# Optimization experiments

Measured on AMD Instinct MI355X. Metric: run time of the kernel, lower is better.

## Reference

```python
import jax, jax.numpy as jnp
import numpy as np

D_MODEL = 1024
N_HEADS = 16
N_KV_HEADS = 4
D_HEAD = D_MODEL // N_HEADS  # 64
GROUP = N_HEADS // N_KV_HEADS  # 4
SCALE = 1.0 / np.sqrt(D_HEAD)
BATCH, SEQ = 2, 2048


def setup_inputs() -> dict:
    key = jax.random.key(0)
    ks = jax.random.split(key, 12)
    w = 0.02
    qkv = jax.random.normal(ks[0], (BATCH, SEQ, D_MODEL), dtype=jnp.float32)
    # RoPE angles: positions * inverse frequencies, shape [SEQ, D_HEAD//2]
    inv_freq = 1.0 / (10000.0 ** (jnp.arange(0, D_HEAD, 2, dtype=jnp.float32) / D_HEAD))
    pos_emb = jnp.arange(SEQ, dtype=jnp.float32)[:, None] * inv_freq[None, :]
    Wq = jax.random.normal(ks[1], (D_MODEL, D_MODEL), dtype=jnp.float32) * w
    bq = jax.random.normal(ks[2], (D_MODEL,), dtype=jnp.float32) * w
    Wk = jax.random.normal(ks[3], (D_MODEL, N_KV_HEADS * D_HEAD), dtype=jnp.float32) * w
    bk = jax.random.normal(ks[4], (N_KV_HEADS * D_HEAD,), dtype=jnp.float32) * w
    Wv = jax.random.normal(ks[5], (D_MODEL, N_KV_HEADS * D_HEAD), dtype=jnp.float32) * w
    bv = jax.random.normal(ks[6], (N_KV_HEADS * D_HEAD,), dtype=jnp.float32) * w
    Wo = jax.random.normal(ks[7], (D_MODEL, D_MODEL), dtype=jnp.float32) * w
    bo = jax.random.normal(ks[8], (D_MODEL,), dtype=jnp.float32) * w
    return {"qkv": qkv, "pos_emb": pos_emb, "Wq": Wq, "bq": bq, "Wk": Wk, "bk": bk,
            "Wv": Wv, "bv": bv, "Wo": Wo, "bo": bo}


def _rotate_half(x):
    x1, x2 = jnp.split(x, 2, axis=-1)
    return jnp.concatenate([-x2, x1], axis=-1)


def _apply_rope(q, k, pos_emb):
    # q: [B,S,H,Dh], k: [B,S,Kv,Dh], pos_emb: [S, Dh/2] angles
    cos = jnp.cos(pos_emb)
    sin = jnp.sin(pos_emb)
    cos = jnp.concatenate([cos, cos], axis=-1)[None, :, None, :]  # [1,S,1,Dh]
    sin = jnp.concatenate([sin, sin], axis=-1)[None, :, None, :]
    q = q * cos + _rotate_half(q) * sin
    k = k * cos + _rotate_half(k) * sin
    return q, k


def reference(qkv, pos_emb, Wq, bq, Wk, bk, Wv, bv, Wo, bo):
    B, S, D = qkv.shape
    q = qkv @ Wq + bq                           # [B,S,D]
    k = qkv @ Wk + bk                           # [B,S,Kv*Dh]
    v = qkv @ Wv + bv
    q = q.reshape(B, S, N_HEADS, D_HEAD)
    k = k.reshape(B, S, N_KV_HEADS, D_HEAD)
    v = v.reshape(B, S, N_KV_HEADS, D_HEAD)
    q, k = _apply_rope(q, k, pos_emb)
    q = q.transpose(0, 2, 1, 3)                 # [B,H,S,Dh]
    k = k.transpose(0, 2, 1, 3)                 # [B,Kv,S,Dh]
    v = v.transpose(0, 2, 1, 3)
    # GQA: replicate each kv head across its query-head group
    k = jnp.repeat(k, GROUP, axis=1)            # [B,H,S,Dh]
    v = jnp.repeat(v, GROUP, axis=1)
    scores = jnp.einsum('bhqd,bhkd->bhqk', q, k) * SCALE
    causal = jnp.tril(jnp.ones((S, S), dtype=bool))
    scores = jnp.where(causal[None, None, :, :], scores, jnp.finfo(scores.dtype).min)
    attn = jax.nn.softmax(scores, axis=-1)
    out = jnp.einsum('bhqk,bhkd->bhqd', attn, v)  # [B,H,S,Dh]
    out = out.transpose(0, 2, 1, 3).reshape(B, S, D)
    return out @ Wo + bo
```

## Files before the change

kernel.cpp:

```cpp
#include <hip/hip_runtime.h>
#include <hip/hip_bf16.h>

using f32x4  = __attribute__((ext_vector_type(4))) float;
using short8 = __attribute__((ext_vector_type(8))) short;
using u16    = unsigned short;
using u32    = unsigned int;

#define B_SZ   2
#define S_LEN  2048
#define NH     16
#define NKV    4
#define DH     64
#define DM     1024
#define NQKVC  1536
#define MROWS  4096
#define QSCALE 0.18033688011112042f

__device__ __forceinline__ u16 f2bf(float f) {
  return __builtin_bit_cast(u16, __float2bfloat16(f));
}
__device__ __forceinline__ float bf2f(u16 b) {
  return __builtin_bit_cast(float, ((u32)b) << 16);
}
__device__ __forceinline__ void gld16(const void* g, void* l) {
  __builtin_amdgcn_global_load_lds((const __attribute__((address_space(1))) u32*)g,
                                   (__attribute__((address_space(3))) u32*)l, 16, 0, 0);
}

__device__ __forceinline__ void transp_tile(const float* __restrict__ w, int ncols,
                                            u16* __restrict__ wt, int bx, int by,
                                            int tid, float (*t)[33]) {
  const int k0 = bx * 32, n0 = by * 32;
  const int tx = tid & 31, ty = tid >> 5;
#pragma unroll
  for (int j = 0; j < 32; j += 8)
    t[ty + j][tx] = w[(size_t)(k0 + ty + j) * ncols + n0 + tx];
  __syncthreads();
#pragma unroll
  for (int j = 0; j < 32; j += 8)
    wt[(size_t)(n0 + ty + j) * 1024 + k0 + tx] = f2bf(t[tx][ty + j]);
}

__global__ __launch_bounds__(256) void k_prep(
    const float* __restrict__ x, u16* __restrict__ xb,
    const float* __restrict__ Wq, const float* __restrict__ Wk,
    const float* __restrict__ Wv, const float* __restrict__ Wo,
    u16* __restrict__ Wqkvt, u16* __restrict__ Wot,
    const float* __restrict__ bq, const float* __restrict__ bk,
    const float* __restrict__ bv, const float* __restrict__ pe,
    float* __restrict__ biasqkv, float* __restrict__ cs, float* __restrict__ sn) {
  __shared__ float tt[32][33];
  const int job = blockIdx.x, tid = threadIdx.x;
  if (job < 1024) {
#pragma unroll
    for (int u = 0; u < 4; ++u) {
      int i = job * 4096 + u * 1024 + tid * 4;
      float4 v = *(const float4*)(x + i);
      ushort4 o;
      o.x = f2bf(v.x); o.y = f2bf(v.y); o.z = f2bf(v.z); o.w = f2bf(v.w);
      *(ushort4*)(xb + i) = o;
    }
  } else if (job < 2048) {
    int t = job - 1024;
    transp_tile(Wq, 1024, Wqkvt, t & 31, t >> 5, tid, tt);
  } else if (job < 2304) {
    int t = job - 2048;
    transp_tile(Wk, 256, Wqkvt + (size_t)1024 * 1024, t & 31, t >> 5, tid, tt);
  } else if (job < 2560) {
    int t = job - 2304;
    transp_tile(Wv, 256, Wqkvt + (size_t)1280 * 1024, t & 31, t >> 5, tid, tt);
  } else if (job < 3584) {
    int t = job - 2560;
    transp_tile(Wo, 1024, Wot, t & 31, t >> 5, tid, tt);
  } else {
    int i = (job - 3584) * 256 + tid;
    if (i < NQKVC)
      biasqkv[i] = (i < 1024) ? bq[i] : (i < 1280 ? bk[i - 1024] : bv[i - 1280]);
    float a = pe[i];
    cs[i] = cosf(a);
    sn[i] = sinf(a);
  }
}

template <typename OUT_T>
__global__ __launch_bounds__(256) void k_gemm(const u16* __restrict__ A,
                                              const u16* __restrict__ Bt,
                                              const float* __restrict__ bias,
                                              OUT_T* __restrict__ C,
                                              int M, int N, int K) {
  __shared__ u16 la[128 * 32];
  __shared__ u16 lb[64 * 32];
  const int tid = threadIdx.x;
  const int m0 = blockIdx.x * 128, n0 = blockIdx.y * 64;
  const int lane = tid & 63, wv = tid >> 6;
  const int g = lane >> 4, lr = lane & 15;
  const int wr = wv >> 1, wc = wv & 1;

  const int sr = tid >> 2;
  const int scol = (tid & 3) * 8;
  const u16* pa0 = A  + (size_t)(m0 + sr) * K + scol;
  const u16* pa1 = A  + (size_t)(m0 + 64 + sr) * K + scol;
  const u16* pb  = Bt + (size_t)(n0 + sr) * K + scol;
  u16* lda0 = &la[wv * 512];
  u16* lda1 = &la[2048 + wv * 512];
  u16* ldb  = &lb[wv * 512];

  f32x4 acc[4][2] = {};
  const int nk = K >> 5;
  for (int kt = 0; kt < nk; ++kt) {
    const int ko = kt * 32;
    gld16(pa0 + ko, lda0);
    gld16(pa1 + ko, lda1);
    gld16(pb + ko, ldb);
    __syncthreads();
    short8 af[4], bfr[2];
#pragma unroll
    for (int m = 0; m < 4; ++m)
      af[m] = *(const short8*)&la[(64 * wr + 16 * m + lr) * 32 + 8 * g];
#pragma unroll
    for (int n = 0; n < 2; ++n)
      bfr[n] = *(const short8*)&lb[(32 * wc + 16 * n + lr) * 32 + 8 * g];
#pragma unroll
    for (int m = 0; m < 4; ++m)
#pragma unroll
      for (int n = 0; n < 2; ++n)
        acc[m][n] = __builtin_amdgcn_mfma_f32_16x16x32_bf16(af[m], bfr[n], acc[m][n], 0, 0, 0);
    __syncthreads();
  }

#pragma unroll
  for (int m = 0; m < 4; ++m)
#pragma unroll
    for (int n = 0; n < 2; ++n) {
      const int col = n0 + 32 * wc + 16 * n + lr;
      const float bz = bias[col];
#pragma unroll
      for (int r = 0; r < 4; ++r) {
        const int row = m0 + 64 * wr + 16 * m + 4 * g + r;
        float v = acc[m][n][r] + bz;
        if constexpr (sizeof(OUT_T) == 2) C[(size_t)row * N + col] = f2bf(v);
        else                              C[(size_t)row * N + col] = v;
      }
    }
}

__global__ __launch_bounds__(256) void k_rv(const u16* __restrict__ p,
                                            const float* __restrict__ cs,
                                            const float* __restrict__ sn,
                                            u16* __restrict__ Qr, u16* __restrict__ Kr,
                                            u16* __restrict__ Vt) {
  __shared__ u16 tt[32][33];
  const int job = blockIdx.x, tid = threadIdx.x;
  if (job < 4096) {
    const int row = job;
    const int b = row >> 11, s = row & 2047;
    const u16* pr = p + (size_t)row * NQKVC;
    const float* crow = cs + s * 32;
    const float* srow = sn + s * 32;
#pragma unroll
    for (int it = 0; it < 4; ++it) {
      int c = it * 256 + tid;
      int h = c >> 6, d = c & 63, j = d & 31;
      float x = bf2f(pr[c]);
      float y = bf2f(pr[c ^ 32]);
      float o = (x * crow[j] + (d < 32 ? -y : y) * srow[j]) * QSCALE;
      Qr[((size_t)(b * NH + h) * S_LEN + s) * DH + d] = f2bf(o);
    }
    {
      int c = 1024 + tid;
      int kvh = tid >> 6, d = tid & 63, j = d & 31;
      float x = bf2f(pr[c]);
      float y = bf2f(pr[c ^ 32]);
      float o = x * crow[j] + (d < 32 ? -y : y) * srow[j];
      Kr[((size_t)(b * NKV + kvh) * S_LEN + s) * DH + d] = f2bf(o);
    }
  } else {
    const int idx = job - 4096;
    const int st = (idx & 63) * 32;
    const int dt = ((idx >> 6) & 1) * 32;
    const int bkv = idx >> 7;
    const int b = bkv >> 2, kv = bkv & 3;
    const int tx = tid & 31, ty = tid >> 5;
#pragma unroll
    for (int j = 0; j < 32; j += 8)
      tt[ty + j][tx] = p[(size_t)(b * S_LEN + st + ty + j) * NQKVC + 1280 + kv * 64 + dt + tx];
    __syncthreads();
#pragma unroll
    for (int j = 0; j < 32; j += 8)
      Vt[((size_t)(b * NKV + kv) * DH + dt + ty + j) * S_LEN + st + tx] = tt[tx][ty + j];
  }
}

__global__ __launch_bounds__(512, 4) void k_attn(const u16* __restrict__ Qr,
                                                 const u16* __restrict__ Kr,
                                                 const u16* __restrict__ Vt,
                                                 u16* __restrict__ Og) {
  __shared__ u16 kbuf[2][4096];
  __shared__ u16 vbuf[2][4096];
  __shared__ u16 plds[8][16][72];

  const int tid = threadIdx.x, wv = tid >> 6, lane = tid & 63;
  const int g = lane >> 4, lr = lane & 15;
  const int wg = blockIdx.x;
  const int xcd = wg & 7, iw = wg >> 3;
  const int bh = xcd * 4 + (iw & 3);
  const int j = iw >> 2;
  const int pr = (j < 8) ? j : 23 - j;
  const int b = bh >> 4, h = bh & 15, kv = h >> 2;
  const int qt = (wv >> 2) ? (31 - pr) : pr;
  const int q0w = qt * 64 + (wv & 3) * 16;
  const int myq = q0w + lr;
  const int myNt = qt + 1;
  const int nt = 32 - pr;

  const u16* Kbase = Kr + (size_t)(b * NKV + kv) * S_LEN * DH;
  const u16* Vbase = Vt + (size_t)(b * NKV + kv) * DH * S_LEN;

  const int sr = tid >> 3;
  const int sc = tid & 7;
  const int ssw = sc ^ (sr & 7);
  const int rsw = lr & 7;
  u16* prow = &plds[wv][lr][0];

  const u16* Qb = Qr + ((size_t)(b * NH + h) * S_LEN + q0w) * DH;
  short8 qf0 = *(const short8*)(Qb + lr * DH + 8 * g);
  short8 qf1 = *(const short8*)(Qb + lr * DH + 32 + 8 * g);

  float m = -1e30f, l = 0.f;
  f32x4 accO[4] = {};
  const f32x4 z = {};

  gld16(Kbase + (size_t)sr * DH + ssw * 8,    &kbuf[0][wv * 512]);
  gld16(Vbase + (size_t)sr * S_LEN + ssw * 8, &vbuf[0][wv * 512]);
  __syncthreads();
  int buf = 0;
  for (int ti = 0; ti < nt; ++ti) {
    const int kb = ti * 64;
    if (ti + 1 < nt) {
      const int kn = kb + 64;
      gld16(Kbase + (size_t)(kn + sr) * DH + ssw * 8,   &kbuf[buf ^ 1][wv * 512]);
      gld16(Vbase + (size_t)sr * S_LEN + kn + ssw * 8,  &vbuf[buf ^ 1][wv * 512]);
    }
    if (ti < myNt) {
      const u16* kl = kbuf[buf];
      const u16* vl = vbuf[buf];
      short8 k0[4], k1[4];
#pragma unroll
      for (int t = 0; t < 4; ++t) {
        const int row = 16 * t + lr;
        k0[t] = *(const short8*)&kl[row * 64 + (g ^ rsw) * 8];
        k1[t] = *(const short8*)&kl[row * 64 + ((4 + g) ^ rsw) * 8];
      }
      f32x4 s[4];
      __builtin_amdgcn_s_setprio(1);
#pragma unroll
      for (int t = 0; t < 4; ++t) {
        s[t] = __builtin_amdgcn_mfma_f32_16x16x32_bf16(k0[t], qf0, z, 0, 0, 0);
        s[t] = __builtin_amdgcn_mfma_f32_16x16x32_bf16(k1[t], qf1, s[t], 0, 0, 0);
      }
      __builtin_amdgcn_s_setprio(0);
      if (kb + 63 > q0w) {
#pragma unroll
        for (int t = 0; t < 4; ++t)
#pragma unroll
          for (int r = 0; r < 4; ++r)
            if (kb + 16 * t + 4 * g + r > myq) s[t][r] = -1e30f;
      }
      float a0 = fmaxf(fmaxf(fmaxf(s[0][0], s[0][1]), s[0][2]), s[0][3]);
      float a1 = fmaxf(fmaxf(fmaxf(s[1][0], s[1][1]), s[1][2]), s[1][3]);
      float a2 = fmaxf(fmaxf(fmaxf(s[2][0], s[2][1]), s[2][2]), s[2][3]);
      float a3 = fmaxf(fmaxf(fmaxf(s[3][0], s[3][1]), s[3][2]), s[3][3]);
      float tm = fmaxf(fmaxf(a0, a1), fmaxf(a2, a3));
      tm = fmaxf(tm, __shfl_xor(tm, 16));
      tm = fmaxf(tm, __shfl_xor(tm, 32));
      if (__any(tm > m + 8.f)) {
        float mn = fmaxf(tm, m);
        float al = __builtin_exp2f(m - mn);
        m = mn;
        l *= al;
#pragma unroll
        for (int t = 0; t < 4; ++t) {
          accO[t][0] *= al; accO[t][1] *= al; accO[t][2] *= al; accO[t][3] *= al;
        }
      }
      float rs = 0.f;
#pragma unroll
      for (int t = 0; t < 4; ++t)
#pragma unroll
        for (int r = 0; r < 4; ++r) {
          float e = __builtin_exp2f(s[t][r] - m);
          s[t][r] = e;
          rs += e;
        }
      rs += __shfl_xor(rs, 16);
      rs += __shfl_xor(rs, 32);
      l += rs;
#pragma unroll
      for (int t = 0; t < 4; ++t) {
        u32 lo = (u32)f2bf(s[t][0]) | ((u32)f2bf(s[t][1]) << 16);
        u32 hi = (u32)f2bf(s[t][2]) | ((u32)f2bf(s[t][3]) << 16);
        uint2 w2; w2.x = lo; w2.y = hi;
        *(uint2*)(prow + 16 * t + 4 * g) = w2;
      }
      short8 pb0 = *(const short8*)(prow + 8 * g);
      short8 pb1 = *(const short8*)(prow + 32 + 8 * g);
      __builtin_amdgcn_s_setprio(1);
#pragma unroll
      for (int t = 0; t < 4; ++t) {
        const int row = 16 * t + lr;
        short8 vf0 = *(const short8*)&vl[row * 64 + (g ^ rsw) * 8];
        short8 vf1 = *(const short8*)&vl[row * 64 + ((4 + g) ^ rsw) * 8];
        accO[t] = __builtin_amdgcn_mfma_f32_16x16x32_bf16(vf0, pb0, accO[t], 0, 0, 0);
        accO[t] = __builtin_amdgcn_mfma_f32_16x16x32_bf16(vf1, pb1, accO[t], 0, 0, 0);
      }
      __builtin_amdgcn_s_setprio(0);
    }
    __syncthreads();
    buf ^= 1;
  }

  const float inv = 1.0f / l;
  u16* orow = Og + ((size_t)(b * S_LEN + q0w + lr)) * DM + h * DH;
#pragma unroll
  for (int t = 0; t < 4; ++t) {
    ushort4 o;
    o.x = f2bf(accO[t][0] * inv);
    o.y = f2bf(accO[t][1] * inv);
    o.z = f2bf(accO[t][2] * inv);
    o.w = f2bf(accO[t][3] * inv);
    *(ushort4*)(orow + 16 * t + 4 * g) = o;
  }
}

extern "C" void kernel_launch(void* const* d_in, const int* in_sizes, int n_in,
                              void* d_out, int out_size, void* d_ws, size_t ws_size,
                              hipStream_t stream) {
  const float* x  = (const float*)d_in[0];
  const float* pe = (const float*)d_in[1];
  const float* Wq = (const float*)d_in[2];
  const float* bq = (const float*)d_in[3];
  const float* Wk = (const float*)d_in[4];
  const float* bk = (const float*)d_in[5];
  const float* Wv = (const float*)d_in[6];
  const float* bv = (const float*)d_in[7];
  const float* Wo = (const float*)d_in[8];
  const float* bo = (const float*)d_in[9];
  float* out = (float*)d_out;

  char* w = (char*)d_ws;
  u16* Xb      = (u16*)w;   w += (size_t)MROWS * DM * 2;
  u16* Wqkvt   = (u16*)w;   w += (size_t)NQKVC * DM * 2;
  u16* Wot     = (u16*)w;   w += (size_t)DM * DM * 2;
  float* biasq = (float*)w; w += NQKVC * 4;
  float* cs    = (float*)w; w += S_LEN * 32 * 4;
  float* sn    = (float*)w; w += S_LEN * 32 * 4;
  u16* QKVp    = (u16*)w;   w += (size_t)MROWS * NQKVC * 2;
  u16* Qr      = (u16*)w;   w += (size_t)B_SZ * NH * S_LEN * DH * 2;
  u16* Kr      = (u16*)w;   w += (size_t)B_SZ * NKV * S_LEN * DH * 2;
  u16* Vt      = (u16*)w;   w += (size_t)B_SZ * NKV * DH * S_LEN * 2;
  u16* Og      = (u16*)w;

  k_prep<<<3840, 256, 0, stream>>>(x, Xb, Wq, Wk, Wv, Wo, Wqkvt, Wot,
                                   bq, bk, bv, pe, biasq, cs, sn);

  k_gemm<u16><<<dim3(MROWS / 128, NQKVC / 64), 256, 0, stream>>>(
      Xb, Wqkvt, biasq, QKVp, MROWS, NQKVC, DM);

  k_rv<<<4096 + 1024, 256, 0, stream>>>(QKVp, cs, sn, Qr, Kr, Vt);

  k_attn<<<512, 512, 0, stream>>>(Qr, Kr, Vt, Og);

  k_gemm<float><<<dim3(MROWS / 128, DM / 64), 256, 0, stream>>>(
      Og, Wot, bo, out, MROWS, DM, DM);
}
```

Baseline: 187.2 us.

## Fuse RoPE and V transpose into QKV GEMM epilogue, double-buffer GEMM LDS

Adds a mode to the GEMM kernel whose epilogue stages the tile in shared memory, applies RoPE and the Q scale, and writes Qr, Kr and transposed Vt directly. This removes the separate rope/transpose kernel and the intermediate QKV buffer round trip. The GEMM main loop also double-buffers LDS, prefetching the next K slice before the MFMAs with one barrier per step. Larger shared memory use may reduce occupancy.

```diff
diff --git a/kernel.cpp b/kernel.cpp
--- a/kernel.cpp
+++ b/kernel.cpp
@@ -82,14 +82,23 @@
   }
 }
 
-template <typename OUT_T>
+template <int MODE, typename OUT_T>
 __global__ __launch_bounds__(256) void k_gemm(const u16* __restrict__ A,
                                               const u16* __restrict__ Bt,
                                               const float* __restrict__ bias,
                                               OUT_T* __restrict__ C,
-                                              int M, int N, int K) {
-  __shared__ u16 la[128 * 32];
-  __shared__ u16 lb[64 * 32];
+                                              int M, int N, int K,
+                                              const float* __restrict__ cs,
+                                              const float* __restrict__ sn,
+                                              u16* __restrict__ Qr,
+                                              u16* __restrict__ Kr,
+                                              u16* __restrict__ Vt) {
+  __shared__ __align__(16) char smraw[33280];
+  u16* laB0 = (u16*)smraw;
+  u16* laB1 = (u16*)smraw + 4096;
+  u16* lbB0 = (u16*)(smraw + 16384);
+  u16* lbB1 = (u16*)(smraw + 16384) + 2048;
+
   const int tid = threadIdx.x;
   const int m0 = blockIdx.x * 128, n0 = blockIdx.y * 64;
   const int lane = tid & 63, wv = tid >> 6;
@@ -101,18 +110,24 @@
   const u16* pa0 = A  + (size_t)(m0 + sr) * K + scol;
   const u16* pa1 = A  + (size_t)(m0 + 64 + sr) * K + scol;
   const u16* pb  = Bt + (size_t)(n0 + sr) * K + scol;
-  u16* lda0 = &la[wv * 512];
-  u16* lda1 = &la[2048 + wv * 512];
-  u16* ldb  = &lb[wv * 512];
 
   f32x4 acc[4][2] = {};
   const int nk = K >> 5;
+  gld16(pa0, laB0 + wv * 512);
+  gld16(pa1, laB0 + 2048 + wv * 512);
+  gld16(pb,  lbB0 + wv * 512);
+  __syncthreads();
   for (int kt = 0; kt < nk; ++kt) {
-    const int ko = kt * 32;
-    gld16(pa0 + ko, lda0);
-    gld16(pa1 + ko, lda1);
-    gld16(pb + ko, ldb);
-    __syncthreads();
+    const u16* la = (kt & 1) ? laB1 : laB0;
+    const u16* lb = (kt & 1) ? lbB1 : lbB0;
+    if (kt + 1 < nk) {
+      u16* lan = (kt & 1) ? laB0 : laB1;
+      u16* lbn = (kt & 1) ? lbB0 : lbB1;
+      const int ko = (kt + 1) * 32;
+      gld16(pa0 + ko, lan + wv * 512);
+      gld16(pa1 + ko, lan + 2048 + wv * 512);
+      gld16(pb + ko,  lbn + wv * 512);
+    }
     short8 af[4], bfr[2];
 #pragma unroll
     for (int m = 0; m < 4; ++m)
@@ -128,66 +143,74 @@
     __syncthreads();
   }
 
-#pragma unroll
-  for (int m = 0; m < 4; ++m)
-#pragma unroll
-    for (int n = 0; n < 2; ++n) {
-      const int col = n0 + 32 * wc + 16 * n + lr;
-      const float bz = bias[col];
-#pragma unroll
-      for (int r = 0; r < 4; ++r) {
-        const int row = m0 + 64 * wr + 16 * m + 4 * g + r;
-        float v = acc[m][n][r] + bz;
-        if constexpr (sizeof(OUT_T) == 2) C[(size_t)row * N + col] = f2bf(v);
-        else                              C[(size_t)row * N + col] = v;
-      }
-    }
-}
-
-__global__ __launch_bounds__(256) void k_rv(const u16* __restrict__ p,
-                                            const float* __restrict__ cs,
-                                            const float* __restrict__ sn,
-                                            u16* __restrict__ Qr, u16* __restrict__ Kr,
-                                            u16* __restrict__ Vt) {
-  __shared__ u16 tt[32][33];
-  const int job = blockIdx.x, tid = threadIdx.x;
-  if (job < 4096) {
-    const int row = job;
-    const int b = row >> 11, s = row & 2047;
-    const u16* pr = p + (size_t)row * NQKVC;
-    const float* crow = cs + s * 32;
-    const float* srow = sn + s * 32;
-#pragma unroll
-    for (int it = 0; it < 4; ++it) {
-      int c = it * 256 + tid;
-      int h = c >> 6, d = c & 63, j = d & 31;
-      float x = bf2f(pr[c]);
-      float y = bf2f(pr[c ^ 32]);
-      float o = (x * crow[j] + (d < 32 ? -y : y) * srow[j]) * QSCALE;
-      Qr[((size_t)(b * NH + h) * S_LEN + s) * DH + d] = f2bf(o);
-    }
-    {
-      int c = 1024 + tid;
-      int kvh = tid >> 6, d = tid & 63, j = d & 31;
-      float x = bf2f(pr[c]);
-      float y = bf2f(pr[c ^ 32]);
-      float o = x * crow[j] + (d < 32 ? -y : y) * srow[j];
-      Kr[((size_t)(b * NKV + kvh) * S_LEN + s) * DH + d] = f2bf(o);
-    }
+  if constexpr (MODE == 0) {
+#pragma unroll
+    for (int m = 0; m < 4; ++m)
+#pragma unroll
+      for (int n = 0; n < 2; ++n) {
+        const int col = n0 + 32 * wc + 16 * n + lr;
+        const float bz = bias[col];
+#pragma unroll
+        for (int r = 0; r < 4; ++r) {
+          const int row = m0 + 64 * wr + 16 * m + 4 * g + r;
+          C[(size_t)row * N + col] = acc[m][n][r] + bz;
+        }
+      }
   } else {
-    const int idx = job - 4096;
-    const int st = (idx & 63) * 32;
-    const int dt = ((idx >> 6) & 1) * 32;
-    const int bkv = idx >> 7;
-    const int b = bkv >> 2, kv = bkv & 3;
-    const int tx = tid & 31, ty = tid >> 5;
-#pragma unroll
-    for (int j = 0; j < 32; j += 8)
-      tt[ty + j][tx] = p[(size_t)(b * S_LEN + st + ty + j) * NQKVC + 1280 + kv * 64 + dt + tx];
+    float (*ct)[65] = (float (*)[65])smraw;
+#pragma unroll
+    for (int m = 0; m < 4; ++m)
+#pragma unroll
+      for (int n = 0; n < 2; ++n) {
+        const int lcol = 32 * wc + 16 * n + lr;
+        const float bz = bias[n0 + lcol];
+#pragma unroll
+        for (int r = 0; r < 4; ++r)
+          ct[64 * wr + 16 * m + 4 * g + r][lcol] = acc[m][n][r] + bz;
+      }
     __syncthreads();
 #pragma unroll
-    for (int j = 0; j < 32; j += 8)
-      Vt[((size_t)(b * NKV + kv) * DH + dt + ty + j) * S_LEN + st + tx] = tt[tx][ty + j];
+    for (int m = 0; m < 4; ++m)
+#pragma unroll
+      for (int n = 0; n < 2; ++n) {
+        const int lcol = 32 * wc + 16 * n + lr;
+        const int c = n0 + lcol;
+        const int lr0 = 64 * wr + 16 * m + 4 * g;
+        const int grow0 = m0 + lr0;
+        const int b = grow0 >> 11;
+        const int s0 = grow0 & 2047;
+        if (c < 1024) {
+          const int h = c >> 6, d = c & 63, j = d & 31;
+          const float sg = (d < 32) ? -1.f : 1.f;
+          u16* qp = Qr + ((size_t)(b * NH + h) * S_LEN + s0) * DH + d;
+#pragma unroll
+          for (int r = 0; r < 4; ++r) {
+            float xv = ct[lr0 + r][lcol];
+            float yv = ct[lr0 + r][lcol ^ 32];
+            float o = (xv * cs[(s0 + r) * 32 + j] + sg * yv * sn[(s0 + r) * 32 + j]) * QSCALE;
+            qp[(size_t)r * DH] = f2bf(o);
+          }
+        } else if (c < 1280) {
+          const int cc = c - 1024, kvh = cc >> 6, d = cc & 63, j = d & 31;
+          const float sg = (d < 32) ? -1.f : 1.f;
+          u16* kp = Kr + ((size_t)(b * NKV + kvh) * S_LEN + s0) * DH + d;
+#pragma unroll
+          for (int r = 0; r < 4; ++r) {
+            float xv = ct[lr0 + r][lcol];
+            float yv = ct[lr0 + r][lcol ^ 32];
+            float o = xv * cs[(s0 + r) * 32 + j] + sg * yv * sn[(s0 + r) * 32 + j];
+            kp[(size_t)r * DH] = f2bf(o);
+          }
+        } else {
+          const int cc = c - 1280, kv = cc >> 6, d = cc & 63;
+          ushort4 o4;
+          o4.x = f2bf(ct[lr0 + 0][lcol]);
+          o4.y = f2bf(ct[lr0 + 1][lcol]);
+          o4.z = f2bf(ct[lr0 + 2][lcol]);
+          o4.w = f2bf(ct[lr0 + 3][lcol]);
+          *(ushort4*)(Vt + ((size_t)(b * NKV + kv) * DH + d) * S_LEN + s0) = o4;
+        }
+      }
   }
 }
 
@@ -354,7 +377,6 @@
   float* biasq = (float*)w; w += NQKVC * 4;
   float* cs    = (float*)w; w += S_LEN * 32 * 4;
   float* sn    = (float*)w; w += S_LEN * 32 * 4;
-  u16* QKVp    = (u16*)w;   w += (size_t)MROWS * NQKVC * 2;
   u16* Qr      = (u16*)w;   w += (size_t)B_SZ * NH * S_LEN * DH * 2;
   u16* Kr      = (u16*)w;   w += (size_t)B_SZ * NKV * S_LEN * DH * 2;
   u16* Vt      = (u16*)w;   w += (size_t)B_SZ * NKV * DH * S_LEN * 2;
@@ -363,13 +385,11 @@
   k_prep<<<3840, 256, 0, stream>>>(x, Xb, Wq, Wk, Wv, Wo, Wqkvt, Wot,
                                    bq, bk, bv, pe, biasq, cs, sn);
 
-  k_gemm<u16><<<dim3(MROWS / 128, NQKVC / 64), 256, 0, stream>>>(
-      Xb, Wqkvt, biasq, QKVp, MROWS, NQKVC, DM);
-
-  k_rv<<<4096 + 1024, 256, 0, stream>>>(QKVp, cs, sn, Qr, Kr, Vt);
+  k_gemm<1, u16><<<dim3(MROWS / 128, NQKVC / 64), 256, 0, stream>>>(
+      Xb, Wqkvt, biasq, (u16*)nullptr, MROWS, NQKVC, DM, cs, sn, Qr, Kr, Vt);
 
   k_attn<<<512, 512, 0, stream>>>(Qr, Kr, Vt, Og);
 
-  k_gemm<float><<<dim3(MROWS / 128, DM / 64), 256, 0, stream>>>(
-      Og, Wot, bo, out, MROWS, DM, DM);
-}
+  k_gemm<0, float><<<dim3(MROWS / 128, DM / 64), 256, 0, stream>>>(
+      Og, Wot, bo, out, MROWS, DM, DM, nullptr, nullptr, nullptr, nullptr, nullptr);
+}
```

Result: faster. 176.8 us (-5.6%).
